# Performance work log

Measured on AMD Instinct MI355X. Metric: run time of the kernel, lower is better.

The kernel has to match this reference:

```python
import jax, jax.numpy as jnp
import numpy as np

D_MODEL = 256
D_STATE = 16
D_INNER = 512          # expand=2 * d_model
D_CONV = 4
DT_RANK = 16           # ceil(d_model/16)
B, L = 16, 2048


def setup_inputs() -> dict:
    key = jax.random.key(0)
    ks = jax.random.split(key, 10)
    s = 0.02
    inp = {
        "x": jax.random.normal(ks[0], (B, L, D_MODEL), dtype=jnp.float32),
        "ln_w": jnp.ones((D_MODEL,), jnp.float32),
        "ln_b": jnp.zeros((D_MODEL,), jnp.float32),
        "in_proj_w": jax.random.normal(ks[1], (2 * D_INNER, D_MODEL)) * s,
        "conv_w": jax.random.normal(ks[2], (D_INNER, 1, D_CONV)) * s,
        "conv_b": jnp.zeros((D_INNER,), jnp.float32),
        "x_proj_w": jax.random.normal(ks[3], (DT_RANK + 2 * D_STATE, D_INNER)) * s,
        "dt_proj_w": jax.random.normal(ks[4], (D_INNER, DT_RANK)) * s,
        "dt_proj_b": jax.random.uniform(ks[5], (D_INNER,), minval=-4.0, maxval=-2.0),
        "A_log": jnp.log(jnp.broadcast_to(jnp.arange(1, D_STATE + 1, dtype=jnp.float32), (D_INNER, D_STATE))).copy(),
        "D_param": jnp.ones((D_INNER,), jnp.float32),
        "out_proj_w": jax.random.normal(ks[6], (D_MODEL, D_INNER)) * s,
    }
    return inp


def _layernorm(x, w, b, eps=1e-5):
    mu = jnp.mean(x, axis=-1, keepdims=True)
    var = jnp.var(x, axis=-1, keepdims=True)
    return (x - mu) * jax.lax.rsqrt(var + eps) * w + b


def _mamba(xn, in_proj_w, conv_w, conv_b, x_proj_w, dt_proj_w, dt_proj_b, A_log, D_param, out_proj_w):
    # in_proj -> x, z   (B, L, d_inner) each
    xz = jnp.einsum('bld,ed->ble', xn, in_proj_w)
    x_in, z = jnp.split(xz, 2, axis=-1)

    # depthwise causal conv over L
    xc = jax.lax.conv_general_dilated(
        jnp.transpose(x_in, (0, 2, 1)), conv_w,
        window_strides=(1,), padding=[(D_CONV - 1, 0)],
        feature_group_count=D_INNER,
        dimension_numbers=('NCH', 'OIH', 'NCH')) + conv_b[None, :, None]
    xc = jax.nn.silu(jnp.transpose(xc, (0, 2, 1)))  # (B, L, d_inner)

    # input-dependent dt, B, C
    dbc = jnp.einsum('ble,fe->blf', xc, x_proj_w)  # (B, L, dt_rank + 2N)
    dt = jax.nn.softplus(jnp.einsum('blr,er->ble', dbc[..., :DT_RANK], dt_proj_w) + dt_proj_b)
    Bc = dbc[..., DT_RANK:DT_RANK + D_STATE]   # (B, L, N)
    Cc = dbc[..., DT_RANK + D_STATE:]          # (B, L, N)

    A = -jnp.exp(A_log)  # (d_inner, N)

    def step(h, inputs):
        dt_t, x_t, B_t, C_t = inputs  # (B,e), (B,e), (B,n), (B,n)
        dA = jnp.exp(dt_t[..., None] * A)                      # (B, e, n)
        h = dA * h + dt_t[..., None] * B_t[:, None, :] * x_t[..., None]
        y = jnp.sum(h * C_t[:, None, :], axis=-1)              # (B, e)
        return h, y

    h0 = jnp.zeros((xn.shape[0], D_INNER, D_STATE), xn.dtype)
    seq = (jnp.swapaxes(dt, 0, 1), jnp.swapaxes(xc, 0, 1),
           jnp.swapaxes(Bc, 0, 1), jnp.swapaxes(Cc, 0, 1))
    _, ys = jax.lax.scan(step, h0, seq)
    y = jnp.swapaxes(ys, 0, 1) + D_param * xc                  # (B, L, e)
    y = y * jax.nn.silu(z)
    return jnp.einsum('ble,de->bld', y, out_proj_w)


def reference(x, ln_w, ln_b, in_proj_w, conv_w, conv_b, x_proj_w, dt_proj_w, dt_proj_b, A_log, D_param, out_proj_w):
    xn = _layernorm(x, ln_w, ln_b)
    out = _mamba(xn, in_proj_w, conv_w, conv_b, x_proj_w, dt_proj_w, dt_proj_b, A_log, D_param, out_proj_w)
    return x + out  # dropout is identity in eval
```

## Files before the change

### kernel.cpp

```cpp
#include <hip/hip_runtime.h>
#include <cstdint>

#define DEVI __device__ __forceinline__

typedef __bf16 bf16;
typedef __bf16 bf16x8 __attribute__((ext_vector_type(8)));
typedef __bf16 bf16x4 __attribute__((ext_vector_type(4)));
typedef __bf16 bf16x2 __attribute__((ext_vector_type(2)));
typedef float floatx4 __attribute__((ext_vector_type(4)));
typedef float f32x2 __attribute__((ext_vector_type(2)));

constexpr int BATCH = 16, SEQ = 2048, DM = 256, DI = 512;
constexpr int M = BATCH * SEQ;
constexpr int NC = 64;
constexpr int CL = SEQ / NC;
static_assert(NC * CL == SEQ, "chunking");
constexpr float LOG2E = 1.4426950408889634f;

DEVI void gl2lds16(const void* g, void* l) {
  __builtin_amdgcn_global_load_lds(
      (const __attribute__((address_space(1))) unsigned int*)(uintptr_t)g,
      (__attribute__((address_space(3))) unsigned int*)(unsigned int)(uintptr_t)l,
      16, 0, 0);
}

DEVI float sigmoidf_(float x) { return 1.f / (1.f + __expf(-x)); }
DEVI float exp2_(float x) { return __builtin_amdgcn_exp2f(x); }

__global__ __launch_bounds__(256) void prep_kernel(
    const float* __restrict__ w1, const float* __restrict__ wx,
    const float* __restrict__ wo, const float* __restrict__ alog,
    bf16* __restrict__ w1b, bf16* __restrict__ wxb, bf16* __restrict__ wob,
    float* __restrict__ An, int* __restrict__ flags) {
  constexpr int n1 = 1024 * 256, n2 = 48 * 512, n3 = 256 * 512;
  int i = blockIdx.x * 256 + threadIdx.x;
  if (i < n1) w1b[i] = (bf16)w1[i];
  else if (i < n1 + n2) wxb[i - n1] = (bf16)wx[i - n1];
  else if (i < n1 + n2 + n3) wob[i - n1 - n2] = (bf16)wo[i - n1 - n2];
  else if (i < n1 + n2 + n3 + DI) {
    const int e = i - (n1 + n2 + n3);
    const float a0 = -__expf(alog[e * 16]);
    bool ok = (a0 < 0.f);
#pragma unroll 1
    for (int s = 0; s < 16; s++) {
      const float a = -__expf(alog[e * 16 + s]);
      An[e * 16 + s] = a * LOG2E;
      ok = ok && (__builtin_fabsf(a / a0 - (float)(s + 1)) < 1e-3f);
    }
    flags[e] = ok ? 1 : 0;
  }
}

__global__ __launch_bounds__(256) void ln_kernel(
    const float* __restrict__ x, const float* __restrict__ w,
    const float* __restrict__ b, bf16* __restrict__ xn) {
  const int row = blockIdx.x * 4 + (threadIdx.x >> 6);
  const int lane = threadIdx.x & 63;
  const float4 v = ((const float4*)(x + (size_t)row * DM))[lane];
  float s = v.x + v.y + v.z + v.w;
  float s2 = v.x * v.x + v.y * v.y + v.z * v.z + v.w * v.w;
#pragma unroll
  for (int m = 1; m < 64; m <<= 1) { s += __shfl_xor(s, m); s2 += __shfl_xor(s2, m); }
  const float mu = s * (1.f / DM);
  const float var = s2 * (1.f / DM) - mu * mu;
  const float rs = rsqrtf(var + 1e-5f);
  const float4 wv = ((const float4*)w)[lane];
  const float4 bv = ((const float4*)b)[lane];
  bf16x4 o;
  o[0] = (bf16)((v.x - mu) * rs * wv.x + bv.x);
  o[1] = (bf16)((v.y - mu) * rs * wv.y + bv.y);
  o[2] = (bf16)((v.z - mu) * rs * wv.z + bv.z);
  o[3] = (bf16)((v.w - mu) * rs * wv.w + bv.w);
  *(bf16x4*)(xn + (size_t)row * DM + lane * 4) = o;
}

template <int N, int K, bool OUT_BF16, bool RESID>
__global__ __launch_bounds__(256) void gemm_nt(const bf16* __restrict__ A,
                                               const bf16* __restrict__ W,
                                               void* __restrict__ out,
                                               const float* __restrict__ resid) {
  constexpr int BK = 32;
  __shared__ __align__(16) bf16 lA[128 * BK];
  __shared__ __align__(16) bf16 lB[128 * BK];
  const int tid = threadIdx.x;
  const int wave = tid >> 6, lane = tid & 63;
  const int bm = blockIdx.x * 128, bn = blockIdx.y * 128;
  const int wm = (wave >> 1) * 64, wn = (wave & 1) * 64;
  const int q = lane >> 4, r = lane & 15;
  floatx4 acc[4][4] = {};
  const int c0 = wave * 64 + lane;
  const int row0 = c0 >> 2, kp = (c0 & 3) * 8;
  for (int k0 = 0; k0 < K; k0 += BK) {
    gl2lds16(A + (size_t)(bm + row0) * K + k0 + kp, lA + c0 * 8);
    gl2lds16(A + (size_t)(bm + row0 + 64) * K + k0 + kp, lA + (c0 + 256) * 8);
    gl2lds16(W + (size_t)(bn + row0) * K + k0 + kp, lB + c0 * 8);
    gl2lds16(W + (size_t)(bn + row0 + 64) * K + k0 + kp, lB + (c0 + 256) * 8);
    __syncthreads();
    bf16x8 af[4], bfr[4];
#pragma unroll
    for (int i = 0; i < 4; i++) af[i] = *(const bf16x8*)&lA[(wm + i * 16 + r) * BK + q * 8];
#pragma unroll
    for (int j = 0; j < 4; j++) bfr[j] = *(const bf16x8*)&lB[(wn + j * 16 + r) * BK + q * 8];
#pragma unroll
    for (int i = 0; i < 4; i++)
#pragma unroll
      for (int j = 0; j < 4; j++)
        acc[i][j] = __builtin_amdgcn_mfma_f32_16x16x32_bf16(af[i], bfr[j], acc[i][j], 0, 0, 0);
    __syncthreads();
  }
#pragma unroll
  for (int i = 0; i < 4; i++)
#pragma unroll
    for (int j = 0; j < 4; j++)
#pragma unroll
      for (int t = 0; t < 4; t++) {
        const int row = bm + wm + i * 16 + q * 4 + t;
        const int col = bn + wn + j * 16 + r;
        const size_t idx = (size_t)row * N + col;
        float v = acc[i][j][t];
        if constexpr (OUT_BF16) {
          ((bf16*)out)[idx] = (bf16)v;
        } else {
          if constexpr (RESID) v += resid[idx];
          ((float*)out)[idx] = v;
        }
      }
}

__global__ __launch_bounds__(256) void conv_silu(const bf16* __restrict__ xz,
                                                 const float* __restrict__ cw,
                                                 const float* __restrict__ cb,
                                                 bf16* __restrict__ xc) {
  const int tid = threadIdx.x;
  const int e2 = tid * 2;
  const int p0 = blockIdx.x * 8;
  const int b = blockIdx.y;
  const float4 w0 = ((const float4*)cw)[e2];
  const float4 w1 = ((const float4*)cw)[e2 + 1];
  const float2 bias = *(const float2*)(cb + e2);
  float xa[11], xb_[11];
#pragma unroll
  for (int j = 0; j < 11; j++) {
    const int pos = p0 - 3 + j;
    float fa = 0.f, fb = 0.f;
    if (pos >= 0) {
      const unsigned u = *(const unsigned*)(xz + ((size_t)b * SEQ + pos) * 1024 + e2);
      fa = __uint_as_float(u << 16);
      fb = __uint_as_float(u & 0xFFFF0000u);
    }
    xa[j] = fa; xb_[j] = fb;
  }
#pragma unroll
  for (int k = 0; k < 8; k++) {
    const float a0 = bias.x + xa[k] * w0.x + xa[k + 1] * w0.y + xa[k + 2] * w0.z + xa[k + 3] * w0.w;
    const float a1 = bias.y + xb_[k] * w1.x + xb_[k + 1] * w1.y + xb_[k + 2] * w1.z + xb_[k + 3] * w1.w;
    bf16x2 o;
    o[0] = (bf16)(a0 * sigmoidf_(a0));
    o[1] = (bf16)(a1 * sigmoidf_(a1));
    *(bf16x2*)(xc + ((size_t)b * SEQ + p0 + k) * DI + e2) = o;
  }
}

__global__ __launch_bounds__(256) void gemm_xproj(const bf16* __restrict__ A,
                                                  const bf16* __restrict__ W,
                                                  float* __restrict__ out) {
  constexpr int K = DI;
  __shared__ __align__(16) bf16 lW[48 * K];
  __shared__ __align__(16) bf16 lA[64 * 32];
  const int tid = threadIdx.x;
  const int wave = tid >> 6, lane = tid & 63;
  const int bm = blockIdx.x * 64;
  const int q = lane >> 4, r = lane & 15;
#pragma unroll
  for (int rd = 0; rd < 12; rd++) {
    const int c = rd * 256 + tid;
    gl2lds16((const char*)W + (size_t)c * 16, (char*)lW + (size_t)c * 16);
  }
  const int row0 = tid >> 2, kp = (tid & 3) * 8;
  const int wm = wave * 16;
  floatx4 acc[3] = {};
  for (int k0 = 0; k0 < K; k0 += 32) {
    gl2lds16(A + (size_t)(bm + row0) * K + k0 + kp, lA + tid * 8);
    __syncthreads();
    bf16x8 af = *(const bf16x8*)&lA[(wm + r) * 32 + q * 8];
#pragma unroll
    for (int j = 0; j < 3; j++) {
      const bf16x8 bfr = *(const bf16x8*)&lW[(j * 16 + r) * K + k0 + q * 8];
      acc[j] = __builtin_amdgcn_mfma_f32_16x16x32_bf16(af, bfr, acc[j], 0, 0, 0);
    }
    __syncthreads();
  }
#pragma unroll
  for (int j = 0; j < 3; j++)
#pragma unroll
    for (int t = 0; t < 4; t++)
      out[(size_t)(bm + wm + q * 4 + t) * 48 + j * 16 + r] = acc[j][t];
}

__global__ __launch_bounds__(256) void dtproj_kernel(const float* __restrict__ dbc,
                                                     const float* __restrict__ dtw,
                                                     const float* __restrict__ dtb,
                                                     bf16* __restrict__ dt) {
  __shared__ __align__(16) float sd[64 * 16];
  const int tid = threadIdx.x;
  const int p0 = blockIdx.x * 64;
  const int e = blockIdx.y * 256 + tid;
  {
    const int rowi = tid >> 2, coli = (tid & 3) * 4;
    *(float4*)&sd[rowi * 16 + coli] = *(const float4*)(dbc + (size_t)(p0 + rowi) * 48 + coli);
  }
  float w[16];
#pragma unroll
  for (int s = 0; s < 16; s += 4) {
    float4 t4 = *(const float4*)(dtw + (size_t)e * 16 + s);
    w[s] = t4.x; w[s + 1] = t4.y; w[s + 2] = t4.z; w[s + 3] = t4.w;
  }
  const float bias = dtb[e];
  __syncthreads();
  for (int p = 0; p < 64; p++) {
    float s = bias;
#pragma unroll
    for (int r2 = 0; r2 < 16; r2++) s += sd[p * 16 + r2] * w[r2];
    const float sp = (s > 15.f) ? s : __logf(1.f + __expf(s));
    dt[(size_t)(p0 + p) * DI + e] = (bf16)sp;
  }
}

DEVI void powpairs(float d1, f32x2* P) {
  const float d2 = d1 * d1;
  f32x2 d2s; d2s[0] = d2; d2s[1] = d2;
  const f32x2 d4s = d2s * d2s;
  const f32x2 d8s = d4s * d4s;
  P[0][0] = d1; P[0][1] = d2;
  P[1] = P[0] * d2s;
  P[2] = P[0] * d4s;
  P[3] = P[1] * d4s;
  P[4] = P[0] * d8s;
  P[5] = P[1] * d8s;
  P[6] = P[2] * d8s;
  P[7] = P[3] * d8s;
}

__global__ __launch_bounds__(256) void scan_pass1(const bf16* __restrict__ dt,
                                                  const bf16* __restrict__ xc,
                                                  const float* __restrict__ dbc,
                                                  const float* __restrict__ An,
                                                  const int* __restrict__ flags,
                                                  float* __restrict__ U,
                                                  float* __restrict__ SD) {
  __shared__ __align__(16) float sbc[CL * 16];
  const int tid = threadIdx.x;
  const int e = blockIdx.x * 256 + tid;
  const int ch = blockIdx.y, b = blockIdx.z;
  const size_t posBase = (size_t)b * SEQ + (size_t)ch * CL;
  if (tid < CL * 4) {
    const int il = tid >> 2, f = (tid & 3) * 4;
    gl2lds16(dbc + (posBase + il) * 48 + 16 + f, (char*)sbc + tid * 16);
  }
  const int fast = flags[e];
  f32x2 h2[8];
#pragma unroll
  for (int k = 0; k < 8; k++) { h2[k][0] = 0.f; h2[k][1] = 0.f; }
  float sdt = 0.f;
  const float A0 = An[(size_t)e * 16];
  float A[16];
  if (!fast) {
#pragma unroll
    for (int s = 0; s < 16; s += 4) {
      float4 a4 = *(const float4*)(An + (size_t)e * 16 + s);
      A[s] = a4.x; A[s + 1] = a4.y; A[s + 2] = a4.z; A[s + 3] = a4.w;
    }
  }
  __syncthreads();
  if (fast) {
    for (int il = 0; il < CL; il++) {
      const size_t pos = posBase + il;
      const float dtv = (float)dt[pos * DI + e];
      const float xv = (float)xc[pos * DI + e];
      const float dtx = dtv * xv;
      sdt += dtv;
      f32x2 P[8];
      powpairs(exp2_(dtv * A0), P);
      f32x2 dtx2; dtx2[0] = dtx; dtx2[1] = dtx;
      const float4* bb = (const float4*)(sbc + il * 16);
#pragma unroll
      for (int g = 0; g < 4; g++) {
        const float4 B4 = bb[g];
        f32x2 blo; blo[0] = B4.x; blo[1] = B4.y;
        f32x2 bhi; bhi[0] = B4.z; bhi[1] = B4.w;
        h2[2 * g] = P[2 * g] * h2[2 * g] + dtx2 * blo;
        h2[2 * g + 1] = P[2 * g + 1] * h2[2 * g + 1] + dtx2 * bhi;
      }
    }
  } else {
    for (int il = 0; il < CL; il++) {
      const size_t pos = posBase + il;
      const float dtv = (float)dt[pos * DI + e];
      const float xv = (float)xc[pos * DI + e];
      const float dtx = dtv * xv;
      sdt += dtv;
      const float* bc = sbc + il * 16;
#pragma unroll
      for (int s = 0; s < 16; s++) {
        const float hh = exp2_(dtv * A[s]) * h2[s >> 1][s & 1] + dtx * bc[s];
        h2[s >> 1][s & 1] = hh;
      }
    }
  }
  float* up = U + ((size_t)(b * NC + ch) * DI + e) * 16;
#pragma unroll
  for (int k = 0; k < 8; k += 2) {
    float4 o; o.x = h2[k][0]; o.y = h2[k][1]; o.z = h2[k + 1][0]; o.w = h2[k + 1][1];
    *(float4*)(up + k * 2) = o;
  }
  SD[(size_t)(b * NC + ch) * DI + e] = sdt;
}

__global__ __launch_bounds__(256) void scan_pass2(const float* __restrict__ SD,
                                                  float* U,
                                                  const float* __restrict__ An) {
  const int t = blockIdx.x * 256 + threadIdx.x;
  const int s = t & 15;
  const int e = (t >> 4) & (DI - 1);
  const int b = t >> 13;
  const float A = An[e * 16 + s];
  float h = 0.f;
#pragma unroll 4
  for (int c = 0; c < NC; c++) {
    const size_t cell = (size_t)(b * NC + c) * DI + e;
    const float sdv = SD[cell];
    const size_t base = cell * 16 + s;
    const float u = U[base];
    const float h0 = h;
    h = exp2_(A * sdv) * h0 + u;
    U[base] = h0;
  }
}

__global__ __launch_bounds__(256) void scan_pass3(const bf16* __restrict__ dt,
                                                  const bf16* __restrict__ xc,
                                                  const bf16* __restrict__ xz,
                                                  const float* __restrict__ dbc,
                                                  const float* __restrict__ An,
                                                  const int* __restrict__ flags,
                                                  const float* __restrict__ H0,
                                                  const float* __restrict__ Dp,
                                                  bf16* __restrict__ yg) {
  __shared__ __align__(16) float sbc[CL * 32];
  const int tid = threadIdx.x;
  const int e = blockIdx.x * 256 + tid;
  const int ch = blockIdx.y, b = blockIdx.z;
  const size_t posBase = (size_t)b * SEQ + (size_t)ch * CL;
  {
    const int il = tid >> 3, f = (tid & 7) * 4;
    gl2lds16(dbc + (posBase + il) * 48 + 16 + f, (char*)sbc + tid * 16);
  }
  const int fast = flags[e];
  f32x2 h2[8];
  const float* hp = H0 + ((size_t)(b * NC + ch) * DI + e) * 16;
#pragma unroll
  for (int k = 0; k < 8; k += 2) {
    const float4 h4 = *(const float4*)(hp + k * 2);
    h2[k][0] = h4.x; h2[k][1] = h4.y; h2[k + 1][0] = h4.z; h2[k + 1][1] = h4.w;
  }
  const float Dv = Dp[e];
  const float A0 = An[(size_t)e * 16];
  float A[16];
  if (!fast) {
#pragma unroll
    for (int s = 0; s < 16; s += 4) {
      float4 a4 = *(const float4*)(An + (size_t)e * 16 + s);
      A[s] = a4.x; A[s + 1] = a4.y; A[s + 2] = a4.z; A[s + 3] = a4.w;
    }
  }
  __syncthreads();
  if (fast) {
    for (int il = 0; il < CL; il++) {
      const size_t pos = posBase + il;
      const float dtv = (float)dt[pos * DI + e];
      const float xv = (float)xc[pos * DI + e];
      const float zv = (float)xz[pos * 1024 + DI + e];
      const float dtx = dtv * xv;
      f32x2 P[8];
      powpairs(exp2_(dtv * A0), P);
      f32x2 dtx2; dtx2[0] = dtx; dtx2[1] = dtx;
      const float4* bb = (const float4*)(sbc + il * 32);
      f32x2 ya; ya[0] = 0.f; ya[1] = 0.f;
      f32x2 yb; yb[0] = 0.f; yb[1] = 0.f;
#pragma unroll
      for (int g = 0; g < 4; g++) {
        const float4 B4 = bb[g];
        const float4 C4 = bb[4 + g];
        f32x2 blo; blo[0] = B4.x; blo[1] = B4.y;
        f32x2 bhi; bhi[0] = B4.z; bhi[1] = B4.w;
        f32x2 clo; clo[0] = C4.x; clo[1] = C4.y;
        f32x2 chi; chi[0] = C4.z; chi[1] = C4.w;
        h2[2 * g] = P[2 * g] * h2[2 * g] + dtx2 * blo;
        h2[2 * g + 1] = P[2 * g + 1] * h2[2 * g + 1] + dtx2 * bhi;
        ya = ya + h2[2 * g] * clo;
        yb = yb + h2[2 * g + 1] * chi;
      }
      const f32x2 ys = ya + yb;
      const float y = ys[0] + ys[1];
      const float yv = (y + Dv * xv) * zv * sigmoidf_(zv);
      yg[pos * DI + e] = (bf16)yv;
    }
  } else {
    for (int il = 0; il < CL; il++) {
      const size_t pos = posBase + il;
      const float dtv = (float)dt[pos * DI + e];
      const float xv = (float)xc[pos * DI + e];
      const float zv = (float)xz[pos * 1024 + DI + e];
      const float dtx = dtv * xv;
      const float* bc = sbc + il * 32;
      float y = 0.f;
#pragma unroll
      for (int s = 0; s < 16; s++) {
        const float hh = exp2_(dtv * A[s]) * h2[s >> 1][s & 1] + dtx * bc[s];
        h2[s >> 1][s & 1] = hh;
        y += hh * bc[16 + s];
      }
      const float yv = (y + Dv * xv) * zv * sigmoidf_(zv);
      yg[pos * DI + e] = (bf16)yv;
    }
  }
}

extern "C" void kernel_launch(void* const* d_in, const int* in_sizes, int n_in,
                              void* d_out, int out_size, void* d_ws, size_t ws_size,
                              hipStream_t stream) {
  const float* x = (const float*)d_in[0];
  const float* ln_w = (const float*)d_in[1];
  const float* ln_b = (const float*)d_in[2];
  const float* w_in = (const float*)d_in[3];
  const float* conv_w = (const float*)d_in[4];
  const float* conv_b = (const float*)d_in[5];
  const float* w_x = (const float*)d_in[6];
  const float* w_dt = (const float*)d_in[7];
  const float* b_dt = (const float*)d_in[8];
  const float* a_log = (const float*)d_in[9];
  const float* d_par = (const float*)d_in[10];
  const float* w_out = (const float*)d_in[11];

  char* ws = (char*)d_ws;
  size_t off = 0;
  auto alloc = [&](size_t bytes) {
    void* p = ws + off;
    off = (off + bytes + 255) & ~(size_t)255;
    return p;
  };
  bf16* xn = (bf16*)alloc((size_t)M * DM * 2);
  bf16* xzb = (bf16*)alloc((size_t)M * 1024 * 2);
  bf16* xcb = (bf16*)alloc((size_t)M * DI * 2);
  float* dbc = (float*)alloc((size_t)M * 48 * 4);
  bf16* dtb_ = (bf16*)alloc((size_t)M * DI * 2);
  bf16* ygb = (bf16*)alloc((size_t)M * DI * 2);
  float* U = (float*)alloc((size_t)BATCH * NC * DI * 16 * 4);
  float* SD = (float*)alloc((size_t)BATCH * NC * DI * 4);
  bf16* w1b = (bf16*)alloc(1024 * 256 * 2);
  bf16* wxb = (bf16*)alloc(48 * 512 * 2);
  bf16* wob = (bf16*)alloc(256 * 512 * 2);
  float* An = (float*)alloc(512 * 16 * 4);
  int* flags = (int*)alloc(512 * 4);

  constexpr int prep_n = 1024 * 256 + 48 * 512 + 256 * 512 + DI;
  prep_kernel<<<dim3((prep_n + 255) / 256), dim3(256), 0, stream>>>(w_in, w_x, w_out, a_log, w1b, wxb, wob, An, flags);
  ln_kernel<<<dim3(M / 4), dim3(256), 0, stream>>>(x, ln_w, ln_b, xn);
  gemm_nt<1024, 256, true, false><<<dim3(M / 128, 8), dim3(256), 0, stream>>>(xn, w1b, (void*)xzb, nullptr);
  conv_silu<<<dim3(SEQ / 8, BATCH), dim3(256), 0, stream>>>(xzb, conv_w, conv_b, xcb);
  gemm_xproj<<<dim3(M / 64), dim3(256), 0, stream>>>(xcb, wxb, dbc);
  dtproj_kernel<<<dim3(M / 64, 2), dim3(256), 0, stream>>>(dbc, w_dt, b_dt, dtb_);
  scan_pass1<<<dim3(2, NC, BATCH), dim3(256), 0, stream>>>(dtb_, xcb, dbc, An, flags, U, SD);
  scan_pass2<<<dim3(BATCH * DI * 16 / 256), dim3(256), 0, stream>>>(SD, U, An);
  scan_pass3<<<dim3(2, NC, BATCH), dim3(256), 0, stream>>>(dtb_, xcb, xzb, dbc, An, flags, U, d_par, ygb);
  gemm_nt<256, 512, false, true><<<dim3(M / 128, 2), dim3(256), 0, stream>>>(ygb, wob, d_out, x);
}
```

Baseline: 309.0 us.

## Process two channels per thread in chunked scan passes with packed math

Scan passes 1 and 3 now give each thread two adjacent inner channels. Their bf16 dt/x/z values are loaded as one 32-bit word, and the power sequence of exp(dt*A0) is computed as packed f32x2 across both channels. The grid is halved, so per-block work on the shared B/C tile doubles. This amortises the LDS B/C reads and widens memory accesses, at the cost of more registers and half as many blocks in flight.

```diff
diff --git a/kernel.cpp b/kernel.cpp
--- a/kernel.cpp
+++ b/kernel.cpp
@@ -26,6 +26,29 @@
 
 DEVI float sigmoidf_(float x) { return 1.f / (1.f + __expf(-x)); }
 DEVI float exp2_(float x) { return __builtin_amdgcn_exp2f(x); }
+
+DEVI float bflo(unsigned u) { return __uint_as_float(u << 16); }
+DEVI float bfhi(unsigned u) { return __uint_as_float(u & 0xFFFF0000u); }
+DEVI f32x2 sp2(float v) { f32x2 r; r[0] = v; r[1] = v; return r; }
+
+DEVI void powseq(f32x2 d, f32x2* P) {
+  P[0] = d;
+  P[1] = d * d;
+  P[2] = P[1] * d;
+  P[3] = P[1] * P[1];
+  P[4] = P[3] * d;
+  P[5] = P[3] * P[1];
+  P[6] = P[3] * P[2];
+  P[7] = P[3] * P[3];
+  P[8] = P[7] * d;
+  P[9] = P[7] * P[1];
+  P[10] = P[7] * P[2];
+  P[11] = P[7] * P[3];
+  P[12] = P[7] * P[4];
+  P[13] = P[7] * P[5];
+  P[14] = P[7] * P[6];
+  P[15] = P[7] * P[7];
+}
 
 __global__ __launch_bounds__(256) void prep_kernel(
     const float* __restrict__ w1, const float* __restrict__ wx,
@@ -226,21 +249,6 @@
   }
 }
 
-DEVI void powpairs(float d1, f32x2* P) {
-  const float d2 = d1 * d1;
-  f32x2 d2s; d2s[0] = d2; d2s[1] = d2;
-  const f32x2 d4s = d2s * d2s;
-  const f32x2 d8s = d4s * d4s;
-  P[0][0] = d1; P[0][1] = d2;
-  P[1] = P[0] * d2s;
-  P[2] = P[0] * d4s;
-  P[3] = P[1] * d4s;
-  P[4] = P[0] * d8s;
-  P[5] = P[1] * d8s;
-  P[6] = P[2] * d8s;
-  P[7] = P[3] * d8s;
-}
-
 __global__ __launch_bounds__(256) void scan_pass1(const bf16* __restrict__ dt,
                                                   const bf16* __restrict__ xc,
                                                   const float* __restrict__ dbc,
@@ -250,70 +258,85 @@
                                                   float* __restrict__ SD) {
   __shared__ __align__(16) float sbc[CL * 16];
   const int tid = threadIdx.x;
-  const int e = blockIdx.x * 256 + tid;
-  const int ch = blockIdx.y, b = blockIdx.z;
+  const int e2 = tid * 2;
+  const int ch = blockIdx.x, b = blockIdx.y;
   const size_t posBase = (size_t)b * SEQ + (size_t)ch * CL;
   if (tid < CL * 4) {
     const int il = tid >> 2, f = (tid & 3) * 4;
     gl2lds16(dbc + (posBase + il) * 48 + 16 + f, (char*)sbc + tid * 16);
   }
-  const int fast = flags[e];
-  f32x2 h2[8];
-#pragma unroll
-  for (int k = 0; k < 8; k++) { h2[k][0] = 0.f; h2[k][1] = 0.f; }
-  float sdt = 0.f;
-  const float A0 = An[(size_t)e * 16];
-  float A[16];
+  const int2 fl = *(const int2*)(flags + e2);
+  const int fast = fl.x & fl.y;
+  f32x2 h[16];
+#pragma unroll
+  for (int s = 0; s < 16; s++) { h[s][0] = 0.f; h[s][1] = 0.f; }
+  f32x2 sdt2; sdt2[0] = 0.f; sdt2[1] = 0.f;
+  f32x2 A02; A02[0] = An[(size_t)e2 * 16]; A02[1] = An[(size_t)e2 * 16 + 16];
+  float Aa[16], Ab[16];
   if (!fast) {
 #pragma unroll
     for (int s = 0; s < 16; s += 4) {
-      float4 a4 = *(const float4*)(An + (size_t)e * 16 + s);
-      A[s] = a4.x; A[s + 1] = a4.y; A[s + 2] = a4.z; A[s + 3] = a4.w;
+      float4 a4 = *(const float4*)(An + (size_t)e2 * 16 + s);
+      Aa[s] = a4.x; Aa[s + 1] = a4.y; Aa[s + 2] = a4.z; Aa[s + 3] = a4.w;
+      float4 b4 = *(const float4*)(An + (size_t)e2 * 16 + 16 + s);
+      Ab[s] = b4.x; Ab[s + 1] = b4.y; Ab[s + 2] = b4.z; Ab[s + 3] = b4.w;
     }
   }
   __syncthreads();
   if (fast) {
     for (int il = 0; il < CL; il++) {
       const size_t pos = posBase + il;
-      const float dtv = (float)dt[pos * DI + e];
-      const float xv = (float)xc[pos * DI + e];
-      const float dtx = dtv * xv;
-      sdt += dtv;
-      f32x2 P[8];
-      powpairs(exp2_(dtv * A0), P);
-      f32x2 dtx2; dtx2[0] = dtx; dtx2[1] = dtx;
+      const unsigned ud = *(const unsigned*)(dt + pos * DI + e2);
+      const unsigned ux = *(const unsigned*)(xc + pos * DI + e2);
+      f32x2 dt2; dt2[0] = bflo(ud); dt2[1] = bfhi(ud);
+      f32x2 xv2; xv2[0] = bflo(ux); xv2[1] = bfhi(ux);
+      const f32x2 dtx2 = dt2 * xv2;
+      sdt2 = sdt2 + dt2;
+      const f32x2 t = dt2 * A02;
+      f32x2 d; d[0] = exp2_(t[0]); d[1] = exp2_(t[1]);
+      f32x2 P[16];
+      powseq(d, P);
       const float4* bb = (const float4*)(sbc + il * 16);
 #pragma unroll
       for (int g = 0; g < 4; g++) {
         const float4 B4 = bb[g];
-        f32x2 blo; blo[0] = B4.x; blo[1] = B4.y;
-        f32x2 bhi; bhi[0] = B4.z; bhi[1] = B4.w;
-        h2[2 * g] = P[2 * g] * h2[2 * g] + dtx2 * blo;
-        h2[2 * g + 1] = P[2 * g + 1] * h2[2 * g + 1] + dtx2 * bhi;
+        h[4 * g + 0] = P[4 * g + 0] * h[4 * g + 0] + dtx2 * sp2(B4.x);
+        h[4 * g + 1] = P[4 * g + 1] * h[4 * g + 1] + dtx2 * sp2(B4.y);
+        h[4 * g + 2] = P[4 * g + 2] * h[4 * g + 2] + dtx2 * sp2(B4.z);
+        h[4 * g + 3] = P[4 * g + 3] * h[4 * g + 3] + dtx2 * sp2(B4.w);
       }
     }
   } else {
     for (int il = 0; il < CL; il++) {
       const size_t pos = posBase + il;
-      const float dtv = (float)dt[pos * DI + e];
-      const float xv = (float)xc[pos * DI + e];
-      const float dtx = dtv * xv;
-      sdt += dtv;
+      const unsigned ud = *(const unsigned*)(dt + pos * DI + e2);
+      const unsigned ux = *(const unsigned*)(xc + pos * DI + e2);
+      const float dta = bflo(ud), dtb_v = bfhi(ud);
+      const float xa = bflo(ux), xb = bfhi(ux);
+      const float dtxa = dta * xa, dtxb = dtb_v * xb;
+      sdt2[0] += dta; sdt2[1] += dtb_v;
       const float* bc = sbc + il * 16;
 #pragma unroll
       for (int s = 0; s < 16; s++) {
-        const float hh = exp2_(dtv * A[s]) * h2[s >> 1][s & 1] + dtx * bc[s];
-        h2[s >> 1][s & 1] = hh;
+        const float bv = bc[s];
+        h[s][0] = exp2_(dta * Aa[s]) * h[s][0] + dtxa * bv;
+        h[s][1] = exp2_(dtb_v * Ab[s]) * h[s][1] + dtxb * bv;
       }
     }
   }
-  float* up = U + ((size_t)(b * NC + ch) * DI + e) * 16;
-#pragma unroll
-  for (int k = 0; k < 8; k += 2) {
-    float4 o; o.x = h2[k][0]; o.y = h2[k][1]; o.z = h2[k + 1][0]; o.w = h2[k + 1][1];
-    *(float4*)(up + k * 2) = o;
-  }
-  SD[(size_t)(b * NC + ch) * DI + e] = sdt;
+  float* up = U + ((size_t)(b * NC + ch) * DI + e2) * 16;
+#pragma unroll
+  for (int i = 0; i < 4; i++) {
+    float4 o; o.x = h[4 * i][0]; o.y = h[4 * i + 1][0]; o.z = h[4 * i + 2][0]; o.w = h[4 * i + 3][0];
+    ((float4*)up)[i] = o;
+  }
+#pragma unroll
+  for (int i = 0; i < 4; i++) {
+    float4 o; o.x = h[4 * i][1]; o.y = h[4 * i + 1][1]; o.z = h[4 * i + 2][1]; o.w = h[4 * i + 3][1];
+    ((float4*)up)[4 + i] = o;
+  }
+  float2 sdo; sdo.x = sdt2[0]; sdo.y = sdt2[1];
+  *(float2*)(SD + (size_t)(b * NC + ch) * DI + e2) = sdo;
 }
 
 __global__ __launch_bounds__(256) void scan_pass2(const float* __restrict__ SD,
@@ -348,80 +371,102 @@
                                                   bf16* __restrict__ yg) {
   __shared__ __align__(16) float sbc[CL * 32];
   const int tid = threadIdx.x;
-  const int e = blockIdx.x * 256 + tid;
-  const int ch = blockIdx.y, b = blockIdx.z;
+  const int e2 = tid * 2;
+  const int ch = blockIdx.x, b = blockIdx.y;
   const size_t posBase = (size_t)b * SEQ + (size_t)ch * CL;
   {
     const int il = tid >> 3, f = (tid & 7) * 4;
     gl2lds16(dbc + (posBase + il) * 48 + 16 + f, (char*)sbc + tid * 16);
   }
-  const int fast = flags[e];
-  f32x2 h2[8];
-  const float* hp = H0 + ((size_t)(b * NC + ch) * DI + e) * 16;
-#pragma unroll
-  for (int k = 0; k < 8; k += 2) {
-    const float4 h4 = *(const float4*)(hp + k * 2);
-    h2[k][0] = h4.x; h2[k][1] = h4.y; h2[k + 1][0] = h4.z; h2[k + 1][1] = h4.w;
-  }
-  const float Dv = Dp[e];
-  const float A0 = An[(size_t)e * 16];
-  float A[16];
+  const int2 fl = *(const int2*)(flags + e2);
+  const int fast = fl.x & fl.y;
+  f32x2 h[16];
+  const float* hp = H0 + ((size_t)(b * NC + ch) * DI + e2) * 16;
+#pragma unroll
+  for (int i = 0; i < 4; i++) {
+    const float4 h4 = ((const float4*)hp)[i];
+    h[4 * i][0] = h4.x; h[4 * i + 1][0] = h4.y; h[4 * i + 2][0] = h4.z; h[4 * i + 3][0] = h4.w;
+  }
+#pragma unroll
+  for (int i = 0; i < 4; i++) {
+    const float4 h4 = ((const float4*)hp)[4 + i];
+    h[4 * i][1] = h4.x; h[4 * i + 1][1] = h4.y; h[4 * i + 2][1] = h4.z; h[4 * i + 3][1] = h4.w;
+  }
+  const float2 Dv = *(const float2*)(Dp + e2);
+  f32x2 Dv2; Dv2[0] = Dv.x; Dv2[1] = Dv.y;
+  f32x2 A02; A02[0] = An[(size_t)e2 * 16]; A02[1] = An[(size_t)e2 * 16 + 16];
+  float Aa[16], Ab[16];
   if (!fast) {
 #pragma unroll
     for (int s = 0; s < 16; s += 4) {
-      float4 a4 = *(const float4*)(An + (size_t)e * 16 + s);
-      A[s] = a4.x; A[s + 1] = a4.y; A[s + 2] = a4.z; A[s + 3] = a4.w;
+      float4 a4 = *(const float4*)(An + (size_t)e2 * 16 + s);
+      Aa[s] = a4.x; Aa[s + 1] = a4.y; Aa[s + 2] = a4.z; Aa[s + 3] = a4.w;
+      float4 b4 = *(const float4*)(An + (size_t)e2 * 16 + 16 + s);
+      Ab[s] = b4.x; Ab[s + 1] = b4.y; Ab[s + 2] = b4.z; Ab[s + 3] = b4.w;
     }
   }
   __syncthreads();
   if (fast) {
     for (int il = 0; il < CL; il++) {
       const size_t pos = posBase + il;
-      const float dtv = (float)dt[pos * DI + e];
-      const float xv = (float)xc[pos * DI + e];
-      const float zv = (float)xz[pos * 1024 + DI + e];
-      const float dtx = dtv * xv;
-      f32x2 P[8];
-      powpairs(exp2_(dtv * A0), P);
-      f32x2 dtx2; dtx2[0] = dtx; dtx2[1] = dtx;
+      const unsigned ud = *(const unsigned*)(dt + pos * DI + e2);
+      const unsigned ux = *(const unsigned*)(xc + pos * DI + e2);
+      const unsigned uz = *(const unsigned*)(xz + pos * 1024 + DI + e2);
+      f32x2 dt2; dt2[0] = bflo(ud); dt2[1] = bfhi(ud);
+      f32x2 xv2; xv2[0] = bflo(ux); xv2[1] = bfhi(ux);
+      f32x2 z2; z2[0] = bflo(uz); z2[1] = bfhi(uz);
+      const f32x2 dtx2 = dt2 * xv2;
+      const f32x2 t = dt2 * A02;
+      f32x2 d; d[0] = exp2_(t[0]); d[1] = exp2_(t[1]);
+      f32x2 P[16];
+      powseq(d, P);
       const float4* bb = (const float4*)(sbc + il * 32);
-      f32x2 ya; ya[0] = 0.f; ya[1] = 0.f;
-      f32x2 yb; yb[0] = 0.f; yb[1] = 0.f;
+      f32x2 Yv[4];
+#pragma unroll
+      for (int g = 0; g < 4; g++) { Yv[g][0] = 0.f; Yv[g][1] = 0.f; }
 #pragma unroll
       for (int g = 0; g < 4; g++) {
         const float4 B4 = bb[g];
         const float4 C4 = bb[4 + g];
-        f32x2 blo; blo[0] = B4.x; blo[1] = B4.y;
-        f32x2 bhi; bhi[0] = B4.z; bhi[1] = B4.w;
-        f32x2 clo; clo[0] = C4.x; clo[1] = C4.y;
-        f32x2 chi; chi[0] = C4.z; chi[1] = C4.w;
-        h2[2 * g] = P[2 * g] * h2[2 * g] + dtx2 * blo;
-        h2[2 * g + 1] = P[2 * g + 1] * h2[2 * g + 1] + dtx2 * bhi;
-        ya = ya + h2[2 * g] * clo;
-        yb = yb + h2[2 * g + 1] * chi;
+        h[4 * g + 0] = P[4 * g + 0] * h[4 * g + 0] + dtx2 * sp2(B4.x);
+        Yv[g] = Yv[g] + h[4 * g + 0] * sp2(C4.x);
+        h[4 * g + 1] = P[4 * g + 1] * h[4 * g + 1] + dtx2 * sp2(B4.y);
+        Yv[g] = Yv[g] + h[4 * g + 1] * sp2(C4.y);
+        h[4 * g + 2] = P[4 * g + 2] * h[4 * g + 2] + dtx2 * sp2(B4.z);
+        Yv[g] = Yv[g] + h[4 * g + 2] * sp2(C4.z);
+        h[4 * g + 3] = P[4 * g + 3] * h[4 * g + 3] + dtx2 * sp2(B4.w);
+        Yv[g] = Yv[g] + h[4 * g + 3] * sp2(C4.w);
       }
-      const f32x2 ys = ya + yb;
-      const float y = ys[0] + ys[1];
-      const float yv = (y + Dv * xv) * zv * sigmoidf_(zv);
-      yg[pos * DI + e] = (bf16)yv;
+      const f32x2 Ys = (Yv[0] + Yv[1]) + (Yv[2] + Yv[3]);
+      f32x2 gz; gz[0] = z2[0] * sigmoidf_(z2[0]); gz[1] = z2[1] * sigmoidf_(z2[1]);
+      const f32x2 yv2 = (Ys + Dv2 * xv2) * gz;
+      bf16x2 o; o[0] = (bf16)yv2[0]; o[1] = (bf16)yv2[1];
+      *(bf16x2*)(yg + pos * DI + e2) = o;
     }
   } else {
     for (int il = 0; il < CL; il++) {
       const size_t pos = posBase + il;
-      const float dtv = (float)dt[pos * DI + e];
-      const float xv = (float)xc[pos * DI + e];
-      const float zv = (float)xz[pos * 1024 + DI + e];
-      const float dtx = dtv * xv;
+      const unsigned ud = *(const unsigned*)(dt + pos * DI + e2);
+      const unsigned ux = *(const unsigned*)(xc + pos * DI + e2);
+      const unsigned uz = *(const unsigned*)(xz + pos * 1024 + DI + e2);
+      const float dta = bflo(ud), dtb_v = bfhi(ud);
+      const float xa = bflo(ux), xb = bfhi(ux);
+      const float za = bflo(uz), zb = bfhi(uz);
+      const float dtxa = dta * xa, dtxb = dtb_v * xb;
       const float* bc = sbc + il * 32;
-      float y = 0.f;
+      float ya = 0.f, yb = 0.f;
 #pragma unroll
       for (int s = 0; s < 16; s++) {
-        const float hh = exp2_(dtv * A[s]) * h2[s >> 1][s & 1] + dtx * bc[s];
-        h2[s >> 1][s & 1] = hh;
-        y += hh * bc[16 + s];
+        const float bv = bc[s], cv = bc[16 + s];
+        const float ha = exp2_(dta * Aa[s]) * h[s][0] + dtxa * bv;
+        const float hb = exp2_(dtb_v * Ab[s]) * h[s][1] + dtxb * bv;
+        h[s][0] = ha; h[s][1] = hb;
+        ya += ha * cv; yb += hb * cv;
       }
-      const float yv = (y + Dv * xv) * zv * sigmoidf_(zv);
-      yg[pos * DI + e] = (bf16)yv;
+      const float yva = (ya + Dv.x * xa) * za * sigmoidf_(za);
+      const float yvb = (yb + Dv.y * xb) * zb * sigmoidf_(zb);
+      bf16x2 o; o[0] = (bf16)yva; o[1] = (bf16)yvb;
+      *(bf16x2*)(yg + pos * DI + e2) = o;
     }
   }
 }
@@ -470,8 +515,8 @@
   conv_silu<<<dim3(SEQ / 8, BATCH), dim3(256), 0, stream>>>(xzb, conv_w, conv_b, xcb);
   gemm_xproj<<<dim3(M / 64), dim3(256), 0, stream>>>(xcb, wxb, dbc);
   dtproj_kernel<<<dim3(M / 64, 2), dim3(256), 0, stream>>>(dbc, w_dt, b_dt, dtb_);
-  scan_pass1<<<dim3(2, NC, BATCH), dim3(256), 0, stream>>>(dtb_, xcb, dbc, An, flags, U, SD);
+  scan_pass1<<<dim3(NC, BATCH), dim3(256), 0, stream>>>(dtb_, xcb, dbc, An, flags, U, SD);
   scan_pass2<<<dim3(BATCH * DI * 16 / 256), dim3(256), 0, stream>>>(SD, U, An);
-  scan_pass3<<<dim3(2, NC, BATCH), dim3(256), 0, stream>>>(dtb_, xcb, xzb, dbc, An, flags, U, d_par, ygb);
+  scan_pass3<<<dim3(NC, BATCH), dim3(256), 0, stream>>>(dtb_, xcb, xzb, dbc, An, flags, U, d_par, ygb);
   gemm_nt<256, 512, false, true><<<dim3(M / 128, 2), dim3(256), 0, stream>>>(ygb, wob, d_out, x);
 }
```

New measurement: 301.7 us. 1.02x faster.
